# Kernel optimization log

Hardware: AMD Instinct MI355X
Metric: run time of the kernel (lower is better)

The kernel has to match this reference:

```python
import jax, jax.numpy as jnp
import numpy as np

N, E, H, G2, R = 50000, 800000, 64, 1024, 5  # nodes, edges, hidden, grid^2, rounds


def setup_inputs() -> dict:
    key = jax.random.key(0)
    ks = jax.random.split(key, 12)
    s = 0.05  # weight scale (xavier-ish)
    w = lambda k, shape: jax.random.normal(k, shape, jnp.float32) * s
    return dict(
        node_features=jax.random.normal(ks[0], (N, 2), jnp.float32),
        edge_attr=jax.random.normal(ks[1], (E, 4), jnp.float32),
        node_enc_W=w(ks[2], (2, H)), node_enc_b=jnp.zeros((H,), jnp.float32),
        edge_enc_W=w(ks[3], (4, H)), edge_enc_b=jnp.zeros((H,), jnp.float32),
        edge_mlp_W=w(ks[4], (R, 3 * H, H)), edge_mlp_b=jnp.zeros((R, H), jnp.float32),
        node_mlp_W=w(ks[5], (R, 2 * H, H)), node_mlp_b=jnp.zeros((R, H), jnp.float32),
        dec_W=w(ks[6], (H, H)), dec_b=jnp.zeros((H,), jnp.float32),
        hm1_W=w(ks[7], (H, H)), hm1_b=jnp.zeros((H,), jnp.float32),
        hm2_W=w(ks[8], (H, G2)), hm2_b=jnp.zeros((G2,), jnp.float32),
        edge_index=jax.random.randint(ks[9], (2, E), 0, N),
    )


def reference(node_features, edge_attr, node_enc_W, node_enc_b, edge_enc_W,
              edge_enc_b, edge_mlp_W, edge_mlp_b, node_mlp_W, node_mlp_b,
              dec_W, dec_b, hm1_W, hm1_b, hm2_W, hm2_b, edge_index):
    n_nodes = node_features.shape[0]
    src, dst = edge_index[0], edge_index[1]
    # encoders
    h = jax.nn.relu(node_features @ node_enc_W + node_enc_b)   # [N, H]
    e = jax.nn.relu(edge_attr @ edge_enc_W + edge_enc_b)       # [E, H]
    # message passing rounds (sum aggregation, mean_aggr=False)
    for r in range(edge_mlp_W.shape[0]):
        m_in = jnp.concatenate([h[src], h[dst], e], axis=-1)   # [E, 3H]
        m = jax.nn.relu(m_in @ edge_mlp_W[r] + edge_mlp_b[r])  # [E, H]
        aggr = jax.ops.segment_sum(m, dst, num_segments=n_nodes)  # [N, H]
        h = jax.nn.relu(jnp.concatenate([h, aggr], axis=-1) @ node_mlp_W[r] + node_mlp_b[r])
        e = m  # updated edge state carried to next round
    embeddings = h @ dec_W + dec_b                              # [N, H]
    logits = jax.nn.relu(embeddings @ hm1_W + hm1_b) @ hm2_W + hm2_b  # [N, G2]
    return embeddings, logits
```

## Files before the change

kernel.cpp:

```cpp
#include <hip/hip_runtime.h>

#define HD 64

typedef __attribute__((ext_vector_type(8))) short bf16x8;
typedef __attribute__((ext_vector_type(4))) float f32x4;

#define MFMA16(a, b, c) __builtin_amdgcn_mfma_f32_16x16x32_bf16(a, b, c, 0, 0, 0)

__device__ __forceinline__ float relu(float x) { return x > 0.f ? x : 0.f; }

__device__ __forceinline__ unsigned short f2bf(float f) {
  unsigned u = __float_as_uint(f);
  u += 0x7fff + ((u >> 16) & 1);
  return (unsigned short)(u >> 16);
}
__device__ __forceinline__ float bf2f(short s) {
  return __uint_as_float(((unsigned)(unsigned short)s) << 16);
}
__device__ __forceinline__ bf16x8 ldbf8(const unsigned short* p) {
  return *reinterpret_cast<const bf16x8*>(p);
}
__device__ __forceinline__ float4 ldf4(const float* p) {
  return *reinterpret_cast<const float4*>(p);
}

__global__ __launch_bounds__(256) void k_wt(const float* __restrict__ in,
                                            unsigned short* __restrict__ out,
                                            int K, int Nc) {
  int total = K * Nc;
  int idx = blockIdx.x * 256 + threadIdx.x;
  int b = blockIdx.y;
  if (idx >= total) return;
  int n = idx / K, k = idx - n * K;
  out[(size_t)b * total + idx] = f2bf(in[(size_t)b * total + (size_t)k * Nc + n]);
}

__global__ __launch_bounds__(256) void k_hist(const int* __restrict__ ei,
                                              int* __restrict__ deg, long long E_) {
  long long eid = (long long)blockIdx.x * 256 + threadIdx.x;
  if (eid >= E_) return;
  atomicAdd(deg + ei[E_ + eid], 1);
}

__global__ __launch_bounds__(1024) void k_scan(const int* __restrict__ deg,
                                               int* __restrict__ cnt, int N_) {
  __shared__ int s[1024];
  int t = threadIdx.x;
  int chunk = (N_ + 1023) / 1024;
  int lo = t * chunk, hi = lo + chunk;
  if (lo > N_) lo = N_;
  if (hi > N_) hi = N_;
  int sum = 0;
  for (int i = lo; i < hi; ++i) sum += deg[i];
  s[t] = sum;
  __syncthreads();
  for (int o = 1; o < 1024; o <<= 1) {
    int v = (t >= o) ? s[t - o] : 0;
    __syncthreads();
    s[t] += v;
    __syncthreads();
  }
  int base = (t == 0) ? 0 : s[t - 1];
  for (int i = lo; i < hi; ++i) {
    cnt[i] = base;
    base += deg[i];
  }
}

__global__ __launch_bounds__(256) void k_scatter(const int* __restrict__ ei,
                                                 int* __restrict__ cnt,
                                                 int4* __restrict__ idx4, long long E_) {
  long long eid = (long long)blockIdx.x * 256 + threadIdx.x;
  if (eid >= E_) return;
  int s = ei[eid], d = ei[E_ + eid];
  int pos = atomicAdd(cnt + d, 1);
  idx4[pos] = make_int4((int)eid, s, d, 0);
}

__global__ __launch_bounds__(256) void k_node_enc(
    const float* __restrict__ nf, const float* __restrict__ W,
    const float* __restrict__ b, unsigned short* __restrict__ h, int N_) {
  int t = blockIdx.x * 256 + threadIdx.x;
  int n = t >> 6, j = t & 63;
  if (n >= N_) return;
  float x0 = nf[(size_t)n * 2 + 0], x1 = nf[(size_t)n * 2 + 1];
  h[t] = f2bf(relu(fmaf(x0, W[j], fmaf(x1, W[HD + j], b[j]))));
}

__global__ __launch_bounds__(256) void k_pre(
    const unsigned short* __restrict__ h, const unsigned short* __restrict__ W12t,
    const float* __restrict__ be0, unsigned short* __restrict__ H12, int ntiles) {
  __shared__ __align__(16) float s[4][16][68];
  int wid = threadIdx.x >> 6, l = threadIdx.x & 63;
  int tile = blockIdx.x * 4 + wid;
  int lr = l & 15, lk = l >> 4;
  if (tile >= ntiles) return;
  int r0 = tile * 16;
  const unsigned short* hp = h + (size_t)(r0 + lr) * HD;
  f32x4 a1[4] = {}, a2[4] = {};
#pragma unroll
  for (int kk = 0; kk < 2; ++kk) {
    bf16x8 a = ldbf8(hp + kk * 32 + lk * 8);
#pragma unroll
    for (int nt = 0; nt < 4; ++nt) {
      bf16x8 b1 = ldbf8(W12t + (size_t)(nt * 16 + lr) * 64 + kk * 32 + lk * 8);
      bf16x8 b2 = ldbf8(W12t + 4096 + (size_t)(nt * 16 + lr) * 64 + kk * 32 + lk * 8);
      a1[nt] = MFMA16(a, b1, a1[nt]);
      a2[nt] = MFMA16(a, b2, a2[nt]);
    }
  }
  int erow = l >> 2, c0 = (l & 3) * 16;
#pragma unroll
  for (int nt = 0; nt < 4; ++nt) {
    float bias = be0[nt * 16 + lr];
#pragma unroll
    for (int i = 0; i < 4; ++i) s[wid][lk * 4 + i][nt * 16 + lr] = a1[nt][i] + bias;
  }
  {
    bf16x8 o0, o1;
#pragma unroll
    for (int j = 0; j < 8; ++j) {
      o0[j] = f2bf(s[wid][erow][c0 + j]);
      o1[j] = f2bf(s[wid][erow][c0 + 8 + j]);
    }
    unsigned short* op = H12 + (size_t)(r0 + erow) * 128 + c0;
    *reinterpret_cast<bf16x8*>(op) = o0;
    *reinterpret_cast<bf16x8*>(op + 8) = o1;
  }
#pragma unroll
  for (int nt = 0; nt < 4; ++nt)
#pragma unroll
    for (int i = 0; i < 4; ++i) s[wid][lk * 4 + i][nt * 16 + lr] = a2[nt][i];
  {
    bf16x8 o0, o1;
#pragma unroll
    for (int j = 0; j < 8; ++j) {
      o0[j] = f2bf(s[wid][erow][c0 + j]);
      o1[j] = f2bf(s[wid][erow][c0 + 8 + j]);
    }
    unsigned short* op = H12 + (size_t)(r0 + erow) * 128 + 64 + c0;
    *reinterpret_cast<bf16x8*>(op) = o0;
    *reinterpret_cast<bf16x8*>(op + 8) = o1;
  }
}

template <bool FUSE_ENC>
__global__ __launch_bounds__(256) void k_edge2(
    unsigned short* __restrict__ e, const unsigned short* __restrict__ H12,
    const int4* __restrict__ idx4, const unsigned short* __restrict__ W3t,
    const float* __restrict__ ea, const float* __restrict__ We,
    const float* __restrict__ be, int netiles, int E_) {
  __shared__ __align__(16) float smf[4][16][68];
  int wid = threadIdx.x >> 6, l = threadIdx.x & 63;
  int tp = blockIdx.x * 4 + wid;
  int lr = l & 15, lk = l >> 4;
  int erow = l >> 2, c0 = (l & 3) * 16;
  int t0 = tp * 2;
  if (t0 >= netiles) return;

  int r0[2] = {t0 * 16, (t0 + 1) * 16};
  bool tv[2] = {true, (t0 + 1) < netiles};

  bf16x8 g1a[2], g1b[2], g2a[2], g2b[2];
#pragma unroll
  for (int u = 0; u < 2; ++u) {
    int4 q = idx4[min(r0[u] + erow, E_ - 1)];
    const unsigned short* h1p = H12 + (size_t)q.y * 128 + c0;
    const unsigned short* h2p = H12 + (size_t)q.z * 128 + 64 + c0;
    g1a[u] = ldbf8(h1p);
    g1b[u] = ldbf8(h1p + 8);
    g2a[u] = ldbf8(h2p);
    g2b[u] = ldbf8(h2p + 8);
  }

  bf16x8 afrag[2][2];
#pragma unroll
  for (int u = 0; u < 2; ++u) {
    int ia = min(r0[u] + lr, E_ - 1);
    if (FUSE_ENC) {
      int eid = idx4[ia].x;
      float4 row = ldf4(ea + (size_t)eid * 4);
#pragma unroll
      for (int kk = 0; kk < 2; ++kk) {
        int j0 = kk * 32 + lk * 8;
        float4 b0 = ldf4(be + j0), b1 = ldf4(be + j0 + 4);
        float v[8] = {b0.x, b0.y, b0.z, b0.w, b1.x, b1.y, b1.z, b1.w};
#pragma unroll
        for (int c = 0; c < 4; ++c) {
          float x = (c == 0) ? row.x : (c == 1) ? row.y : (c == 2) ? row.z : row.w;
          float4 w0 = ldf4(We + c * 64 + j0), w1 = ldf4(We + c * 64 + j0 + 4);
          v[0] = fmaf(x, w0.x, v[0]); v[1] = fmaf(x, w0.y, v[1]);
          v[2] = fmaf(x, w0.z, v[2]); v[3] = fmaf(x, w0.w, v[3]);
          v[4] = fmaf(x, w1.x, v[4]); v[5] = fmaf(x, w1.y, v[5]);
          v[6] = fmaf(x, w1.z, v[6]); v[7] = fmaf(x, w1.w, v[7]);
        }
#pragma unroll
        for (int q = 0; q < 8; ++q) afrag[u][kk][q] = (short)f2bf(relu(v[q]));
      }
    } else {
      const unsigned short* ep = e + (size_t)ia * HD;
      afrag[u][0] = ldbf8(ep + lk * 8);
      afrag[u][1] = ldbf8(ep + 32 + lk * 8);
    }
  }

  f32x4 acc0[4] = {}, acc1[4] = {};
#pragma unroll
  for (int kk = 0; kk < 2; ++kk) {
#pragma unroll
    for (int nt = 0; nt < 4; ++nt) {
      bf16x8 bb = ldbf8(W3t + (size_t)(nt * 16 + lr) * 64 + kk * 32 + lk * 8);
      acc0[nt] = MFMA16(afrag[0][kk], bb, acc0[nt]);
      acc1[nt] = MFMA16(afrag[1][kk], bb, acc1[nt]);
    }
  }

#pragma unroll
  for (int u = 0; u < 2; ++u) {
    if (!tv[u]) continue;
#pragma unroll
    for (int nt = 0; nt < 4; ++nt)
#pragma unroll
      for (int i = 0; i < 4; ++i)
        smf[wid][lk * 4 + i][nt * 16 + lr] = (u == 0) ? acc0[nt][i] : acc1[nt][i];
    float g1f[16], g2f[16];
#pragma unroll
    for (int j = 0; j < 8; ++j) {
      g1f[j] = bf2f(g1a[u][j]); g1f[8 + j] = bf2f(g1b[u][j]);
      g2f[j] = bf2f(g2a[u][j]); g2f[8 + j] = bf2f(g2b[u][j]);
    }
    bf16x8 o0, o1;
#pragma unroll
    for (int q = 0; q < 4; ++q) {
      float4 s4 = ldf4(&smf[wid][erow][c0 + q * 4]);
      float v0 = relu(s4.x + g1f[q * 4 + 0] + g2f[q * 4 + 0]);
      float v1 = relu(s4.y + g1f[q * 4 + 1] + g2f[q * 4 + 1]);
      float v2 = relu(s4.z + g1f[q * 4 + 2] + g2f[q * 4 + 2]);
      float v3 = relu(s4.w + g1f[q * 4 + 3] + g2f[q * 4 + 3]);
      if (q < 2) {
        o0[q * 4 + 0] = f2bf(v0); o0[q * 4 + 1] = f2bf(v1);
        o0[q * 4 + 2] = f2bf(v2); o0[q * 4 + 3] = f2bf(v3);
      } else {
        o1[(q - 2) * 4 + 0] = f2bf(v0); o1[(q - 2) * 4 + 1] = f2bf(v1);
        o1[(q - 2) * 4 + 2] = f2bf(v2); o1[(q - 2) * 4 + 3] = f2bf(v3);
      }
    }
    size_t eb = ((size_t)r0[u] + erow) * HD + c0;
    *reinterpret_cast<bf16x8*>(&e[eb]) = o0;
    *reinterpret_cast<bf16x8*>(&e[eb + 8]) = o1;
  }
}

__global__ __launch_bounds__(256) void k_node_csr(
    unsigned short* __restrict__ h, const unsigned short* __restrict__ m,
    const int* __restrict__ cnt,
    const unsigned short* __restrict__ Wt, const float* __restrict__ b,
    const unsigned short* __restrict__ W12t,
    const float* __restrict__ be_next,
    unsigned short* __restrict__ H12, int ntiles) {
  __shared__ __align__(16) float smf[4][16][68];
  int wid = threadIdx.x >> 6, l = threadIdx.x & 63;
  int tile = blockIdx.x * 4 + wid;
  if (tile >= ntiles) return;
  int r0 = tile * 16;
  int lr = l & 15, lk = l >> 4;

  int node = r0 + lr;
  int q16 = lk * 16;
  int beg = (node == 0) ? 0 : cnt[node - 1];
  int end = cnt[node];
  float s0[16];
#pragma unroll
  for (int j = 0; j < 16; ++j) s0[j] = 0.f;
  for (int i = beg; i < end; ++i) {
    const unsigned short* mp = m + (size_t)i * HD + q16;
    bf16x8 v0 = ldbf8(mp);
    bf16x8 v1 = ldbf8(mp + 8);
#pragma unroll
    for (int j = 0; j < 8; ++j) {
      s0[j] += bf2f(v0[j]);
      s0[8 + j] += bf2f(v1[j]);
    }
  }
#pragma unroll
  for (int j = 0; j < 16; ++j) smf[wid][lr][q16 + j] = s0[j];

  bf16x8 aagg[2];
#pragma unroll
  for (int kk = 0; kk < 2; ++kk) {
    const float* sp = &smf[wid][lr][kk * 32 + lk * 8];
    float4 f0 = ldf4(sp), f1 = ldf4(sp + 4);
    aagg[kk][0] = f2bf(f0.x); aagg[kk][1] = f2bf(f0.y);
    aagg[kk][2] = f2bf(f0.z); aagg[kk][3] = f2bf(f0.w);
    aagg[kk][4] = f2bf(f1.x); aagg[kk][5] = f2bf(f1.y);
    aagg[kk][6] = f2bf(f1.z); aagg[kk][7] = f2bf(f1.w);
  }

  f32x4 acc[4] = {};
#pragma unroll
  for (int kk = 0; kk < 4; ++kk) {
    bf16x8 a = (kk < 2) ? ldbf8(h + (size_t)(r0 + lr) * HD + kk * 32 + lk * 8)
                        : aagg[kk - 2];
#pragma unroll
    for (int nt = 0; nt < 4; ++nt) {
      bf16x8 bb = ldbf8(Wt + (size_t)(kk >> 1) * 4096 +
                        (size_t)(nt * 16 + lr) * 64 + (kk & 1) * 32 + lk * 8);
      acc[nt] = MFMA16(a, bb, acc[nt]);
    }
  }

#pragma unroll
  for (int nt = 0; nt < 4; ++nt) {
    float bias = b[nt * 16 + lr];
#pragma unroll
    for (int i = 0; i < 4; ++i)
      smf[wid][lk * 4 + i][nt * 16 + lr] = relu(acc[nt][i] + bias);
  }
  int erow = l >> 2, c0 = (l & 3) * 16;
  {
    bf16x8 o0, o1;
#pragma unroll
    for (int j = 0; j < 8; ++j) {
      o0[j] = f2bf(smf[wid][erow][c0 + j]);
      o1[j] = f2bf(smf[wid][erow][c0 + 8 + j]);
    }
    size_t hb = (size_t)(r0 + erow) * HD + c0;
    *reinterpret_cast<bf16x8*>(&h[hb]) = o0;
    *reinterpret_cast<bf16x8*>(&h[hb + 8]) = o1;
  }

  if (!W12t) return;

  bf16x8 ah[2];
#pragma unroll
  for (int kk = 0; kk < 2; ++kk) {
    const float* sp = &smf[wid][lr][kk * 32 + lk * 8];
    float4 f0 = ldf4(sp), f1 = ldf4(sp + 4);
    ah[kk][0] = f2bf(f0.x); ah[kk][1] = f2bf(f0.y);
    ah[kk][2] = f2bf(f0.z); ah[kk][3] = f2bf(f0.w);
    ah[kk][4] = f2bf(f1.x); ah[kk][5] = f2bf(f1.y);
    ah[kk][6] = f2bf(f1.z); ah[kk][7] = f2bf(f1.w);
  }
  f32x4 a1[4] = {}, a2[4] = {};
#pragma unroll
  for (int kk = 0; kk < 2; ++kk) {
#pragma unroll
    for (int nt = 0; nt < 4; ++nt) {
      bf16x8 b1 = ldbf8(W12t + (size_t)(nt * 16 + lr) * 64 + kk * 32 + lk * 8);
      bf16x8 b2 = ldbf8(W12t + 4096 + (size_t)(nt * 16 + lr) * 64 + kk * 32 + lk * 8);
      a1[nt] = MFMA16(ah[kk], b1, a1[nt]);
      a2[nt] = MFMA16(ah[kk], b2, a2[nt]);
    }
  }
#pragma unroll
  for (int nt = 0; nt < 4; ++nt) {
    float bias = be_next[nt * 16 + lr];
#pragma unroll
    for (int i = 0; i < 4; ++i)
      smf[wid][lk * 4 + i][nt * 16 + lr] = a1[nt][i] + bias;
  }
  {
    bf16x8 o0, o1;
#pragma unroll
    for (int j = 0; j < 8; ++j) {
      o0[j] = f2bf(smf[wid][erow][c0 + j]);
      o1[j] = f2bf(smf[wid][erow][c0 + 8 + j]);
    }
    unsigned short* op = H12 + (size_t)(r0 + erow) * 128 + c0;
    *reinterpret_cast<bf16x8*>(op) = o0;
    *reinterpret_cast<bf16x8*>(op + 8) = o1;
  }
#pragma unroll
  for (int nt = 0; nt < 4; ++nt)
#pragma unroll
    for (int i = 0; i < 4; ++i)
      smf[wid][lk * 4 + i][nt * 16 + lr] = a2[nt][i];
  {
    bf16x8 o0, o1;
#pragma unroll
    for (int j = 0; j < 8; ++j) {
      o0[j] = f2bf(smf[wid][erow][c0 + j]);
      o1[j] = f2bf(smf[wid][erow][c0 + 8 + j]);
    }
    unsigned short* op = H12 + (size_t)(r0 + erow) * 128 + 64 + c0;
    *reinterpret_cast<bf16x8*>(op) = o0;
    *reinterpret_cast<bf16x8*>(op + 8) = o1;
  }
}

__global__ __launch_bounds__(256) void k_gemm64(
    const unsigned short* __restrict__ Ab, const float* __restrict__ Af,
    const unsigned short* __restrict__ Wt, const float* __restrict__ b,
    float* __restrict__ outf, unsigned short* __restrict__ outb,
    int do_relu, int ntiles) {
  int wid = threadIdx.x >> 6, l = threadIdx.x & 63;
  int tile = blockIdx.x * 4 + wid;
  if (tile >= ntiles) return;
  int r0 = tile * 16;
  int lr = l & 15, lk = l >> 4;

  f32x4 acc[4] = {};
#pragma unroll
  for (int kk = 0; kk < 2; ++kk) {
    bf16x8 a;
    int off = kk * 32 + lk * 8;
    if (Af) {
      const float* ap = Af + (size_t)(r0 + lr) * HD + off;
      float4 f0 = ldf4(ap);
      float4 f1 = ldf4(ap + 4);
      a[0] = f2bf(f0.x); a[1] = f2bf(f0.y); a[2] = f2bf(f0.z); a[3] = f2bf(f0.w);
      a[4] = f2bf(f1.x); a[5] = f2bf(f1.y); a[6] = f2bf(f1.z); a[7] = f2bf(f1.w);
    } else {
      a = ldbf8(Ab + (size_t)(r0 + lr) * HD + off);
    }
#pragma unroll
    for (int nt = 0; nt < 4; ++nt) {
      bf16x8 bb = ldbf8(Wt + (size_t)(nt * 16 + lr) * HD + off);
      acc[nt] = MFMA16(a, bb, acc[nt]);
    }
  }
#pragma unroll
  for (int nt = 0; nt < 4; ++nt) {
    int col = nt * 16 + lr;
    float bias = b[col];
#pragma unroll
    for (int i = 0; i < 4; ++i) {
      float v = acc[nt][i] + bias;
      if (do_relu) v = relu(v);
      size_t o = (size_t)(r0 + lk * 4 + i) * HD + col;
      if (outf) outf[o] = v;
      if (outb) outb[o] = f2bf(v);
    }
  }
}

__global__ __launch_bounds__(256) void k_head_mfma(
    const unsigned short* __restrict__ A, const unsigned short* __restrict__ Wt,
    const float* __restrict__ b2, float* __restrict__ out) {
  __shared__ __align__(16) float sf[4][16][68];
  int wid = threadIdx.x >> 6, l = threadIdx.x & 63;
  int task = blockIdx.x * 4 + wid;
  int mt = task >> 4, ng = task & 15;
  int r0 = mt * 16, n0 = ng * 64;
  int lr = l & 15, lk = l >> 4;

  f32x4 acc[4] = {};
#pragma unroll
  for (int kk = 0; kk < 2; ++kk) {
    bf16x8 a = ldbf8(A + (size_t)(r0 + lr) * HD + kk * 32 + lk * 8);
#pragma unroll
    for (int nt = 0; nt < 4; ++nt) {
      bf16x8 bb = ldbf8(Wt + (size_t)(n0 + nt * 16 + lr) * HD + kk * 32 + lk * 8);
      acc[nt] = MFMA16(a, bb, acc[nt]);
    }
  }
#pragma unroll
  for (int nt = 0; nt < 4; ++nt) {
    int col = nt * 16 + lr;
    float bias = b2[n0 + col];
#pragma unroll
    for (int i = 0; i < 4; ++i) sf[wid][lk * 4 + i][col] = acc[nt][i] + bias;
  }
  int row = l >> 2, cb = (l & 3) * 16;
  float* op = out + (size_t)(r0 + row) * 1024 + n0 + cb;
#pragma unroll
  for (int q = 0; q < 4; ++q)
    *reinterpret_cast<float4*>(op + q * 4) = ldf4(&sf[wid][row][cb + q * 4]);
}

extern "C" void kernel_launch(void* const* d_in, const int* in_sizes, int n_in,
                              void* d_out, int out_size, void* d_ws, size_t ws_size,
                              hipStream_t stream) {
  const float* node_features = (const float*)d_in[0];
  const float* edge_attr     = (const float*)d_in[1];
  const float* node_enc_W    = (const float*)d_in[2];
  const float* node_enc_b    = (const float*)d_in[3];
  const float* edge_enc_W    = (const float*)d_in[4];
  const float* edge_enc_b    = (const float*)d_in[5];
  const float* edge_mlp_W    = (const float*)d_in[6];
  const float* edge_mlp_b    = (const float*)d_in[7];
  const float* node_mlp_W    = (const float*)d_in[8];
  const float* node_mlp_b    = (const float*)d_in[9];
  const float* dec_W         = (const float*)d_in[10];
  const float* dec_b         = (const float*)d_in[11];
  const float* hm1_W         = (const float*)d_in[12];
  const float* hm1_b         = (const float*)d_in[13];
  const float* hm2_W         = (const float*)d_in[14];
  const float* hm2_b         = (const float*)d_in[15];
  const int*   edge_index    = (const int*)d_in[16];

  const int N_ = in_sizes[0] / 2;
  const long long E_ = in_sizes[1] / 4;
  const int R_ = in_sizes[7] / HD;

  char* p = (char*)d_ws;
  unsigned short* e_bf = (unsigned short*)p; p += (size_t)E_ * HD * 2;
  unsigned short* h_bf = (unsigned short*)p; p += (size_t)N_ * HD * 2;
  unsigned short* H12  = (unsigned short*)p; p += (size_t)N_ * 128 * 2;
  unsigned short* t_bf = (unsigned short*)p; p += (size_t)N_ * HD * 2;
  unsigned short* wt_edge = (unsigned short*)p; p += (size_t)R_ * 3 * 64 * 64 * 2;
  unsigned short* wt_node = (unsigned short*)p; p += (size_t)R_ * 2 * 64 * 64 * 2;
  unsigned short* wt_dec = (unsigned short*)p;  p += 64 * 64 * 2;
  unsigned short* wt_hm1 = (unsigned short*)p;  p += 64 * 64 * 2;
  unsigned short* wt_hm2 = (unsigned short*)p;  p += 1024 * 64 * 2;
  int4* idx4 = (int4*)p; p += (size_t)E_ * 16;
  int* deg   = (int*)p; p += (size_t)N_ * 4;
  int* cnt   = (int*)p; p += (size_t)N_ * 4;

  k_wt<<<dim3((64 * 64 + 255) / 256, 3 * R_), 256, 0, stream>>>(edge_mlp_W, wt_edge, 64, 64);
  k_wt<<<dim3((64 * 64 + 255) / 256, 2 * R_), 256, 0, stream>>>(node_mlp_W, wt_node, 64, 64);
  k_wt<<<dim3((64 * 64 + 255) / 256, 1), 256, 0, stream>>>(dec_W, wt_dec, 64, 64);
  k_wt<<<dim3((64 * 64 + 255) / 256, 1), 256, 0, stream>>>(hm1_W, wt_hm1, 64, 64);
  k_wt<<<dim3((64 * 1024 + 255) / 256, 1), 256, 0, stream>>>(hm2_W, wt_hm2, 64, 1024);

  const int e_blocks = (int)((E_ + 255) / 256);
  hipMemsetAsync(deg, 0, (size_t)N_ * 4, stream);
  k_hist<<<e_blocks, 256, 0, stream>>>(edge_index, deg, E_);
  k_scan<<<1, 1024, 0, stream>>>(deg, cnt, N_);
  k_scatter<<<e_blocks, 256, 0, stream>>>(edge_index, cnt, idx4, E_);

  const int nh_blocks = (int)(((size_t)N_ * HD + 255) / 256);
  k_node_enc<<<nh_blocks, 256, 0, stream>>>(node_features, node_enc_W, node_enc_b, h_bf, N_);

  const int netiles = (int)((E_ + 15) / 16);
  const int npairs = (netiles + 1) / 2;
  const int pe_blocks = (npairs + 3) / 4;
  const int ntiles = (N_ + 15) / 16;
  const int nblocks = (ntiles + 3) / 4;

  k_pre<<<nblocks, 256, 0, stream>>>(h_bf, wt_edge, edge_mlp_b, H12, ntiles);

  for (int r = 0; r < R_; ++r) {
    const unsigned short* W3t = wt_edge + (size_t)r * 3 * 4096 + 2 * 4096;
    if (r == 0) {
      k_edge2<true><<<pe_blocks, 256, 0, stream>>>(
          e_bf, H12, idx4, W3t, edge_attr, edge_enc_W, edge_enc_b, netiles, (int)E_);
    } else {
      k_edge2<false><<<pe_blocks, 256, 0, stream>>>(
          e_bf, H12, idx4, W3t, nullptr, nullptr, nullptr, netiles, (int)E_);
    }
    const unsigned short* w12_next =
        (r + 1 < R_) ? (wt_edge + (size_t)(r + 1) * 3 * 4096) : nullptr;
    const float* be_next = edge_mlp_b + (size_t)(r + 1 < R_ ? r + 1 : 0) * HD;
    k_node_csr<<<nblocks, 256, 0, stream>>>(
        h_bf, e_bf, cnt, wt_node + (size_t)r * 2 * 4096,
        node_mlp_b + (size_t)r * HD, w12_next, be_next, H12, ntiles);
  }

  float* out_emb = (float*)d_out;
  float* out_log = out_emb + (size_t)N_ * HD;
  k_gemm64<<<nblocks, 256, 0, stream>>>(h_bf, nullptr, wt_dec, dec_b, out_emb, nullptr, 0, ntiles);
  k_gemm64<<<nblocks, 256, 0, stream>>>(nullptr, out_emb, wt_hm1, hm1_b, nullptr, t_bf, 1, ntiles);
  k_head_mfma<<<ntiles * 4, 256, 0, stream>>>(t_bf, wt_hm2, hm2_b, out_log);
}
```

Before: 776.5 us.

## Fuse last-round aggregation into edge kernel, merge decoder GEMMs, nontemporal head stores

In the final message-passing round the edge kernel no longer writes messages to memory. It reduces them per destination run inside each tile and atomically adds the sums into an fp32 aggregate buffer, which the node kernel then reads instead of walking the CSR. The decoder and hm1 GEMMs are merged into one kernel that keeps embeddings in LDS, and the large logits output uses nontemporal stores. These changes save one edge-tensor write and read plus one launch and intermediate pass, at the cost of a memset, scattered atomics and nondeterministic fp32 summation order.

Measured after the change: 977.0 us. 1.26x slower.

```diff
diff --git a/kernel.cpp b/kernel.cpp
--- a/kernel.cpp
+++ b/kernel.cpp
@@ -144,12 +144,13 @@
   }
 }
 
-template <bool FUSE_ENC>
+template <bool FUSE_ENC, bool LAST>
 __global__ __launch_bounds__(256) void k_edge2(
     unsigned short* __restrict__ e, const unsigned short* __restrict__ H12,
     const int4* __restrict__ idx4, const unsigned short* __restrict__ W3t,
     const float* __restrict__ ea, const float* __restrict__ We,
-    const float* __restrict__ be, int netiles, int E_) {
+    const float* __restrict__ be, float* __restrict__ aggr,
+    int netiles, int E_) {
   __shared__ __align__(16) float smf[4][16][68];
   int wid = threadIdx.x >> 6, l = threadIdx.x & 63;
   int tp = blockIdx.x * 4 + wid;
@@ -215,6 +216,8 @@
     }
   }
 
+  float segsum = 0.f;
+  int prev = LAST ? idx4[r0[0]].z : 0;
 #pragma unroll
   for (int u = 0; u < 2; ++u) {
     if (!tv[u]) continue;
@@ -229,26 +232,45 @@
       g1f[j] = bf2f(g1a[u][j]); g1f[8 + j] = bf2f(g1b[u][j]);
       g2f[j] = bf2f(g2a[u][j]); g2f[8 + j] = bf2f(g2b[u][j]);
     }
-    bf16x8 o0, o1;
+    float v[16];
 #pragma unroll
     for (int q = 0; q < 4; ++q) {
       float4 s4 = ldf4(&smf[wid][erow][c0 + q * 4]);
-      float v0 = relu(s4.x + g1f[q * 4 + 0] + g2f[q * 4 + 0]);
-      float v1 = relu(s4.y + g1f[q * 4 + 1] + g2f[q * 4 + 1]);
-      float v2 = relu(s4.z + g1f[q * 4 + 2] + g2f[q * 4 + 2]);
-      float v3 = relu(s4.w + g1f[q * 4 + 3] + g2f[q * 4 + 3]);
-      if (q < 2) {
-        o0[q * 4 + 0] = f2bf(v0); o0[q * 4 + 1] = f2bf(v1);
-        o0[q * 4 + 2] = f2bf(v2); o0[q * 4 + 3] = f2bf(v3);
-      } else {
-        o1[(q - 2) * 4 + 0] = f2bf(v0); o1[(q - 2) * 4 + 1] = f2bf(v1);
-        o1[(q - 2) * 4 + 2] = f2bf(v2); o1[(q - 2) * 4 + 3] = f2bf(v3);
+      v[q * 4 + 0] = relu(s4.x + g1f[q * 4 + 0] + g2f[q * 4 + 0]);
+      v[q * 4 + 1] = relu(s4.y + g1f[q * 4 + 1] + g2f[q * 4 + 1]);
+      v[q * 4 + 2] = relu(s4.z + g1f[q * 4 + 2] + g2f[q * 4 + 2]);
+      v[q * 4 + 3] = relu(s4.w + g1f[q * 4 + 3] + g2f[q * 4 + 3]);
+    }
+    if (!LAST) {
+      bf16x8 o0, o1;
+#pragma unroll
+      for (int j = 0; j < 8; ++j) {
+        o0[j] = f2bf(v[j]);
+        o1[j] = f2bf(v[8 + j]);
       }
-    }
-    size_t eb = ((size_t)r0[u] + erow) * HD + c0;
-    *reinterpret_cast<bf16x8*>(&e[eb]) = o0;
-    *reinterpret_cast<bf16x8*>(&e[eb + 8]) = o1;
-  }
+      size_t eb = ((size_t)r0[u] + erow) * HD + c0;
+      *reinterpret_cast<bf16x8*>(&e[eb]) = o0;
+      *reinterpret_cast<bf16x8*>(&e[eb + 8]) = o1;
+    } else {
+#pragma unroll
+      for (int q = 0; q < 4; ++q)
+        *reinterpret_cast<float4*>(&smf[wid][erow][c0 + q * 4]) =
+            make_float4(v[q * 4], v[q * 4 + 1], v[q * 4 + 2], v[q * 4 + 3]);
+#pragma unroll
+      for (int r = 0; r < 16; ++r) {
+        int i = r0[u] + r;
+        if (i >= E_) break;
+        int dc = idx4[i].z;
+        if (dc != prev) {
+          atomicAdd(aggr + (size_t)prev * HD + l, segsum);
+          segsum = 0.f;
+          prev = dc;
+        }
+        segsum += smf[wid][r][l];
+      }
+    }
+  }
+  if (LAST) atomicAdd(aggr + (size_t)prev * HD + l, segsum);
 }
 
 __global__ __launch_bounds__(256) void k_node_csr(
@@ -257,7 +279,9 @@
     const unsigned short* __restrict__ Wt, const float* __restrict__ b,
     const unsigned short* __restrict__ W12t,
     const float* __restrict__ be_next,
-    unsigned short* __restrict__ H12, int ntiles) {
+    unsigned short* __restrict__ H12,
+    const float* __restrict__ aggr_in,
+    int ntiles) {
   __shared__ __align__(16) float smf[4][16][68];
   int wid = threadIdx.x >> 6, l = threadIdx.x & 63;
   int tile = blockIdx.x * 4 + wid;
@@ -265,35 +289,46 @@
   int r0 = tile * 16;
   int lr = l & 15, lk = l >> 4;
 
-  int node = r0 + lr;
-  int q16 = lk * 16;
-  int beg = (node == 0) ? 0 : cnt[node - 1];
-  int end = cnt[node];
-  float s0[16];
-#pragma unroll
-  for (int j = 0; j < 16; ++j) s0[j] = 0.f;
-  for (int i = beg; i < end; ++i) {
-    const unsigned short* mp = m + (size_t)i * HD + q16;
-    bf16x8 v0 = ldbf8(mp);
-    bf16x8 v1 = ldbf8(mp + 8);
-#pragma unroll
-    for (int j = 0; j < 8; ++j) {
-      s0[j] += bf2f(v0[j]);
-      s0[8 + j] += bf2f(v1[j]);
-    }
-  }
-#pragma unroll
-  for (int j = 0; j < 16; ++j) smf[wid][lr][q16 + j] = s0[j];
-
   bf16x8 aagg[2];
-#pragma unroll
-  for (int kk = 0; kk < 2; ++kk) {
-    const float* sp = &smf[wid][lr][kk * 32 + lk * 8];
-    float4 f0 = ldf4(sp), f1 = ldf4(sp + 4);
-    aagg[kk][0] = f2bf(f0.x); aagg[kk][1] = f2bf(f0.y);
-    aagg[kk][2] = f2bf(f0.z); aagg[kk][3] = f2bf(f0.w);
-    aagg[kk][4] = f2bf(f1.x); aagg[kk][5] = f2bf(f1.y);
-    aagg[kk][6] = f2bf(f1.z); aagg[kk][7] = f2bf(f1.w);
+  if (aggr_in) {
+#pragma unroll
+    for (int kk = 0; kk < 2; ++kk) {
+      const float* ap = aggr_in + (size_t)(r0 + lr) * HD + kk * 32 + lk * 8;
+      float4 f0 = ldf4(ap), f1 = ldf4(ap + 4);
+      aagg[kk][0] = f2bf(f0.x); aagg[kk][1] = f2bf(f0.y);
+      aagg[kk][2] = f2bf(f0.z); aagg[kk][3] = f2bf(f0.w);
+      aagg[kk][4] = f2bf(f1.x); aagg[kk][5] = f2bf(f1.y);
+      aagg[kk][6] = f2bf(f1.z); aagg[kk][7] = f2bf(f1.w);
+    }
+  } else {
+    int node = r0 + lr;
+    int q16 = lk * 16;
+    int beg = (node == 0) ? 0 : cnt[node - 1];
+    int end = cnt[node];
+    float s0[16];
+#pragma unroll
+    for (int j = 0; j < 16; ++j) s0[j] = 0.f;
+    for (int i = beg; i < end; ++i) {
+      const unsigned short* mp = m + (size_t)i * HD + q16;
+      bf16x8 v0 = ldbf8(mp);
+      bf16x8 v1 = ldbf8(mp + 8);
+#pragma unroll
+      for (int j = 0; j < 8; ++j) {
+        s0[j] += bf2f(v0[j]);
+        s0[8 + j] += bf2f(v1[j]);
+      }
+    }
+#pragma unroll
+    for (int j = 0; j < 16; ++j) smf[wid][lr][q16 + j] = s0[j];
+#pragma unroll
+    for (int kk = 0; kk < 2; ++kk) {
+      const float* sp = &smf[wid][lr][kk * 32 + lk * 8];
+      float4 f0 = ldf4(sp), f1 = ldf4(sp + 4);
+      aagg[kk][0] = f2bf(f0.x); aagg[kk][1] = f2bf(f0.y);
+      aagg[kk][2] = f2bf(f0.z); aagg[kk][3] = f2bf(f0.w);
+      aagg[kk][4] = f2bf(f1.x); aagg[kk][5] = f2bf(f1.y);
+      aagg[kk][6] = f2bf(f1.z); aagg[kk][7] = f2bf(f1.w);
+    }
   }
 
   f32x4 acc[4] = {};
@@ -388,49 +423,76 @@
   }
 }
 
-__global__ __launch_bounds__(256) void k_gemm64(
-    const unsigned short* __restrict__ Ab, const float* __restrict__ Af,
-    const unsigned short* __restrict__ Wt, const float* __restrict__ b,
-    float* __restrict__ outf, unsigned short* __restrict__ outb,
-    int do_relu, int ntiles) {
+__global__ __launch_bounds__(256) void k_dec_hm1(
+    const unsigned short* __restrict__ h,
+    const unsigned short* __restrict__ Wdec, const float* __restrict__ bdec,
+    const unsigned short* __restrict__ Whm1, const float* __restrict__ bhm1,
+    float* __restrict__ emb, unsigned short* __restrict__ t_bf, int ntiles) {
+  __shared__ __align__(16) float smf[4][16][68];
   int wid = threadIdx.x >> 6, l = threadIdx.x & 63;
   int tile = blockIdx.x * 4 + wid;
   if (tile >= ntiles) return;
   int r0 = tile * 16;
   int lr = l & 15, lk = l >> 4;
+  int erow = l >> 2, c0 = (l & 3) * 16;
 
   f32x4 acc[4] = {};
 #pragma unroll
   for (int kk = 0; kk < 2; ++kk) {
-    bf16x8 a;
-    int off = kk * 32 + lk * 8;
-    if (Af) {
-      const float* ap = Af + (size_t)(r0 + lr) * HD + off;
-      float4 f0 = ldf4(ap);
-      float4 f1 = ldf4(ap + 4);
-      a[0] = f2bf(f0.x); a[1] = f2bf(f0.y); a[2] = f2bf(f0.z); a[3] = f2bf(f0.w);
-      a[4] = f2bf(f1.x); a[5] = f2bf(f1.y); a[6] = f2bf(f1.z); a[7] = f2bf(f1.w);
-    } else {
-      a = ldbf8(Ab + (size_t)(r0 + lr) * HD + off);
-    }
+    bf16x8 a = ldbf8(h + (size_t)(r0 + lr) * HD + kk * 32 + lk * 8);
 #pragma unroll
     for (int nt = 0; nt < 4; ++nt) {
-      bf16x8 bb = ldbf8(Wt + (size_t)(nt * 16 + lr) * HD + off);
+      bf16x8 bb = ldbf8(Wdec + (size_t)(nt * 16 + lr) * HD + kk * 32 + lk * 8);
       acc[nt] = MFMA16(a, bb, acc[nt]);
     }
   }
 #pragma unroll
   for (int nt = 0; nt < 4; ++nt) {
-    int col = nt * 16 + lr;
-    float bias = b[col];
-#pragma unroll
-    for (int i = 0; i < 4; ++i) {
-      float v = acc[nt][i] + bias;
-      if (do_relu) v = relu(v);
-      size_t o = (size_t)(r0 + lk * 4 + i) * HD + col;
-      if (outf) outf[o] = v;
-      if (outb) outb[o] = f2bf(v);
-    }
+    float bias = bdec[nt * 16 + lr];
+#pragma unroll
+    for (int i = 0; i < 4; ++i)
+      smf[wid][lk * 4 + i][nt * 16 + lr] = acc[nt][i] + bias;
+  }
+#pragma unroll
+  for (int q = 0; q < 4; ++q)
+    *reinterpret_cast<float4*>(emb + (size_t)(r0 + erow) * HD + c0 + q * 4) =
+        ldf4(&smf[wid][erow][c0 + q * 4]);
+  bf16x8 ah[2];
+#pragma unroll
+  for (int kk = 0; kk < 2; ++kk) {
+    const float* sp = &smf[wid][lr][kk * 32 + lk * 8];
+    float4 f0 = ldf4(sp), f1 = ldf4(sp + 4);
+    ah[kk][0] = f2bf(f0.x); ah[kk][1] = f2bf(f0.y);
+    ah[kk][2] = f2bf(f0.z); ah[kk][3] = f2bf(f0.w);
+    ah[kk][4] = f2bf(f1.x); ah[kk][5] = f2bf(f1.y);
+    ah[kk][6] = f2bf(f1.z); ah[kk][7] = f2bf(f1.w);
+  }
+  f32x4 acc2[4] = {};
+#pragma unroll
+  for (int kk = 0; kk < 2; ++kk) {
+#pragma unroll
+    for (int nt = 0; nt < 4; ++nt) {
+      bf16x8 bb = ldbf8(Whm1 + (size_t)(nt * 16 + lr) * HD + kk * 32 + lk * 8);
+      acc2[nt] = MFMA16(ah[kk], bb, acc2[nt]);
+    }
+  }
+#pragma unroll
+  for (int nt = 0; nt < 4; ++nt) {
+    float bias = bhm1[nt * 16 + lr];
+#pragma unroll
+    for (int i = 0; i < 4; ++i)
+      smf[wid][lk * 4 + i][nt * 16 + lr] = relu(acc2[nt][i] + bias);
+  }
+  {
+    bf16x8 o0, o1;
+#pragma unroll
+    for (int j = 0; j < 8; ++j) {
+      o0[j] = f2bf(smf[wid][erow][c0 + j]);
+      o1[j] = f2bf(smf[wid][erow][c0 + 8 + j]);
+    }
+    size_t tb = (size_t)(r0 + erow) * HD + c0;
+    *reinterpret_cast<bf16x8*>(&t_bf[tb]) = o0;
+    *reinterpret_cast<bf16x8*>(&t_bf[tb + 8]) = o1;
   }
 }
 
@@ -464,8 +526,10 @@
   int row = l >> 2, cb = (l & 3) * 16;
   float* op = out + (size_t)(r0 + row) * 1024 + n0 + cb;
 #pragma unroll
-  for (int q = 0; q < 4; ++q)
-    *reinterpret_cast<float4*>(op + q * 4) = ldf4(&sf[wid][row][cb + q * 4]);
+  for (int q = 0; q < 4; ++q) {
+    f32x4 vv = *reinterpret_cast<const f32x4*>(&sf[wid][row][cb + q * 4]);
+    __builtin_nontemporal_store(vv, reinterpret_cast<f32x4*>(op + q * 4));
+  }
 }
 
 extern "C" void kernel_launch(void* const* d_in, const int* in_sizes, int n_in,
@@ -498,6 +562,7 @@
   unsigned short* h_bf = (unsigned short*)p; p += (size_t)N_ * HD * 2;
   unsigned short* H12  = (unsigned short*)p; p += (size_t)N_ * 128 * 2;
   unsigned short* t_bf = (unsigned short*)p; p += (size_t)N_ * HD * 2;
+  float* aggr = (float*)p;                   p += (size_t)N_ * HD * 4;
   unsigned short* wt_edge = (unsigned short*)p; p += (size_t)R_ * 3 * 64 * 64 * 2;
   unsigned short* wt_node = (unsigned short*)p; p += (size_t)R_ * 2 * 64 * 64 * 2;
   unsigned short* wt_dec = (unsigned short*)p;  p += 64 * 64 * 2;
@@ -532,24 +597,33 @@
 
   for (int r = 0; r < R_; ++r) {
     const unsigned short* W3t = wt_edge + (size_t)r * 3 * 4096 + 2 * 4096;
-    if (r == 0) {
-      k_edge2<true><<<pe_blocks, 256, 0, stream>>>(
-          e_bf, H12, idx4, W3t, edge_attr, edge_enc_W, edge_enc_b, netiles, (int)E_);
-    } else {
-      k_edge2<false><<<pe_blocks, 256, 0, stream>>>(
-          e_bf, H12, idx4, W3t, nullptr, nullptr, nullptr, netiles, (int)E_);
-    }
+    bool fuse = (r == 0), last = (r == R_ - 1);
+    if (last) hipMemsetAsync(aggr, 0, (size_t)N_ * HD * 4, stream);
+    if (fuse && last)
+      k_edge2<true, true><<<pe_blocks, 256, 0, stream>>>(
+          e_bf, H12, idx4, W3t, edge_attr, edge_enc_W, edge_enc_b, aggr, netiles, (int)E_);
+    else if (fuse)
+      k_edge2<true, false><<<pe_blocks, 256, 0, stream>>>(
+          e_bf, H12, idx4, W3t, edge_attr, edge_enc_W, edge_enc_b, nullptr, netiles, (int)E_);
+    else if (last)
+      k_edge2<false, true><<<pe_blocks, 256, 0, stream>>>(
+          e_bf, H12, idx4, W3t, nullptr, nullptr, nullptr, aggr, netiles, (int)E_);
+    else
+      k_edge2<false, false><<<pe_blocks, 256, 0, stream>>>(
+          e_bf, H12, idx4, W3t, nullptr, nullptr, nullptr, nullptr, netiles, (int)E_);
+
     const unsigned short* w12_next =
         (r + 1 < R_) ? (wt_edge + (size_t)(r + 1) * 3 * 4096) : nullptr;
     const float* be_next = edge_mlp_b + (size_t)(r + 1 < R_ ? r + 1 : 0) * HD;
     k_node_csr<<<nblocks, 256, 0, stream>>>(
         h_bf, e_bf, cnt, wt_node + (size_t)r * 2 * 4096,
-        node_mlp_b + (size_t)r * HD, w12_next, be_next, H12, ntiles);
+        node_mlp_b + (size_t)r * HD, w12_next, be_next, H12,
+        last ? aggr : nullptr, ntiles);
   }
 
   float* out_emb = (float*)d_out;
   float* out_log = out_emb + (size_t)N_ * HD;
-  k_gemm64<<<nblocks, 256, 0, stream>>>(h_bf, nullptr, wt_dec, dec_b, out_emb, nullptr, 0, ntiles);
-  k_gemm64<<<nblocks, 256, 0, stream>>>(nullptr, out_emb, wt_hm1, hm1_b, nullptr, t_bf, 1, ntiles);
+  k_dec_hm1<<<nblocks, 256, 0, stream>>>(h_bf, wt_dec, dec_b, wt_hm1, hm1_b,
+                                         out_emb, t_bf, ntiles);
   k_head_mfma<<<ntiles * 4, 256, 0, stream>>>(t_bf, wt_hm2, hm2_b, out_log);
 }
```
